# Kernel tuning notes

Measured on AMD Instinct MI355X. Metric: run time of the kernel, lower is better.

The kernel has to match this reference:

```python
import jax, jax.numpy as jnp
import numpy as np

N, E, H, IN, B, L, OUT = 50000, 600000, 128, 128, 256, 4, 10
BN_EPS = 1e-5


def setup_inputs() -> dict:
    key = jax.random.key(0)
    ks = jax.random.split(key, 12)
    x = jax.random.normal(ks[0], (N, IN), dtype=jnp.float32)
    edge_index = jax.random.randint(ks[1], (2, E), 0, N, dtype=jnp.int64)
    batch = jnp.sort(jax.random.randint(ks[2], (N,), 0, B, dtype=jnp.int64))
    s_in = 1.0 / np.sqrt(IN)
    s_h = 1.0 / np.sqrt(H)
    W_enc = jax.random.uniform(ks[3], (IN, H), jnp.float32, -s_in, s_in)
    b_enc = jax.random.uniform(ks[4], (H,), jnp.float32, -s_in, s_in)
    W = jax.random.uniform(ks[5], (L, H, H), jnp.float32, -s_h, s_h)
    b = jax.random.uniform(ks[6], (L, H), jnp.float32, -s_h, s_h)
    gamma = jnp.ones((L, H), jnp.float32)
    beta = jnp.zeros((L, H), jnp.float32)
    W_cls = jax.random.uniform(ks[7], (H, OUT), jnp.float32, -s_h, s_h)
    b_cls = jax.random.uniform(ks[8], (OUT,), jnp.float32, -s_h, s_h)
    return {"x": x, "edge_index": edge_index, "batch": batch,
            "W_enc": W_enc, "b_enc": b_enc, "W": W, "b": b,
            "gamma": gamma, "beta": beta, "W_cls": W_cls, "b_cls": b_cls}


def reference(x, edge_index, batch, W_enc, b_enc, W, b, gamma, beta, W_cls, b_cls):
    n = x.shape[0]
    # add self-loops (PyG GCNConv default)
    loop = jnp.arange(n, dtype=edge_index.dtype)
    row = jnp.concatenate([edge_index[0], loop])  # source nodes
    col = jnp.concatenate([edge_index[1], loop])  # target nodes
    # symmetric normalization: deg over targets, norm_e = d^-1/2[src] * d^-1/2[dst]
    deg = jax.ops.segment_sum(jnp.ones_like(col, dtype=x.dtype), col, num_segments=n)
    dinv = jnp.where(deg > 0, jax.lax.rsqrt(deg), 0.0)
    norm = dinv[row] * dinv[col]  # [E+N]

    # encoder (plain Linear since use_atom_encoder=False)
    h = x @ W_enc + b_enc

    for l in range(L):
        # GCNConv: transform, normalized scatter-add, bias
        t = h @ W[l]
        msg = norm[:, None] * t[row]               # [E+N, H] gather
        agg = jax.ops.segment_sum(msg, col, num_segments=n) + b[l]
        # BatchNorm1d (batch statistics, training-mode math)
        mean = jnp.mean(agg, axis=0)
        var = jnp.var(agg, axis=0)
        hn = (agg - mean) * jax.lax.rsqrt(var + BN_EPS) * gamma[l] + beta[l]
        h = jax.nn.relu(hn)  # dropout p=0.0 -> identity

    # global mean pool over graphs
    sums = jax.ops.segment_sum(h, batch, num_segments=B)
    counts = jax.ops.segment_sum(jnp.ones((n,), h.dtype), batch, num_segments=B)
    g = sums / jnp.maximum(counts, 1.0)[:, None]
    return g @ W_cls + b_cls
```

## Files before the change

### kernel.cpp

```cpp
#include <hip/hip_runtime.h>

#define NN 50000
#define NE 600000
#define HD 128
#define NL 4
#define NB 256
#define NO 10
#define BN_EPS 1e-5f

typedef short bf16x8 __attribute__((ext_vector_type(8)));
typedef float f32x4 __attribute__((ext_vector_type(4)));

__device__ __forceinline__ unsigned short f2bf(float f) {
    union { float f; unsigned int u; } x; x.f = f;
    unsigned int u = x.u;
    unsigned int r = (u + 0x7FFFu + ((u >> 16) & 1u)) >> 16;
    return (unsigned short)r;
}
__device__ __forceinline__ float bf2f(unsigned short s) {
    union { unsigned int u; float f; } x; x.u = ((unsigned int)s) << 16;
    return x.f;
}


__global__ void hist_kernel(const int* __restrict__ col, int* __restrict__ cnt, int e) {
    int i = blockIdx.x * blockDim.x + threadIdx.x;
    if (i < e) atomicAdd(&cnt[col[i]], 1);
}

__global__ void scan1_kernel(const int* __restrict__ cnt, int* __restrict__ outp,
                             int* __restrict__ bsums, float* __restrict__ dinv,
                             int M, int n) {
    __shared__ int s[256];
    int tid = threadIdx.x;
    int base = blockIdx.x * 1024 + tid * 4;
    int v[4];
#pragma unroll
    for (int j = 0; j < 4; ++j) {
        int idx = base + j;
        v[j] = (idx < n) ? cnt[idx] : 0;
        if (idx < n) dinv[idx] = rsqrtf((float)(v[j] + 1));
    }
    int tot = v[0] + v[1] + v[2] + v[3];
    s[tid] = tot;
    __syncthreads();
    for (int off = 1; off < 256; off <<= 1) {
        int x = (tid >= off) ? s[tid - off] : 0;
        __syncthreads();
        s[tid] += x;
        __syncthreads();
    }
    int run = (tid == 0) ? 0 : s[tid - 1];
#pragma unroll
    for (int j = 0; j < 4; ++j) {
        int idx = base + j;
        if (idx < M) outp[idx] = run;
        run += v[j];
    }
    if (tid == 255) bsums[blockIdx.x] = s[255];
}

__global__ void scan2_kernel(int* bsums, int nb) {
    if (threadIdx.x == 0 && blockIdx.x == 0) {
        int acc = 0;
        for (int i = 0; i < nb; ++i) { int v = bsums[i]; bsums[i] = acc; acc += v; }
    }
}

__global__ void scan3_kernel(int* __restrict__ outp, const int* __restrict__ bsums, int M) {
    int i = blockIdx.x * blockDim.x + threadIdx.x;
    if (i < M) outp[i] += bsums[i >> 10];
}

__global__ void place_kernel(const int* __restrict__ row, const int* __restrict__ col,
                             const float* __restrict__ dinv, const int* __restrict__ rp,
                             int* __restrict__ fill, int2* __restrict__ csr, int e) {
    int i = blockIdx.x * blockDim.x + threadIdx.x;
    if (i < e) {
        int r = row[i], c = col[i];
        int pos = atomicAdd(&fill[c], 1);
        int idx = rp[c] + pos;
        csr[idx] = make_int2(r, __float_as_int(dinv[r] * dinv[c]));
    }
}

__global__ void wconv_kernel(const float* __restrict__ W_enc, const float* __restrict__ W,
                             unsigned short* __restrict__ Wt) {
    int i = blockIdx.x * blockDim.x + threadIdx.x;
    if (i >= 5 * 16384) return;
    int m = i >> 14;
    int r = (i >> 7) & 127;
    int k = i & 127;
    const float* src = (m == 0) ? W_enc : (W + (size_t)(m - 1) * 16384);
    Wt[i] = f2bf(src[k * 128 + r]);
}

template <int AMODE>
__global__ __launch_bounds__(256) void gemm128_mfma(const void* __restrict__ Ap,
                                                    const unsigned short* __restrict__ Wt,
                                                    const float* __restrict__ bias,
                                                    const float* __restrict__ bnp,
                                                    unsigned short* __restrict__ Cp,
                                                    int nrows) {
    int wave = threadIdx.x >> 6;
    int lane = threadIdx.x & 63;
    int r16 = lane & 15;
    int kg = lane >> 4;
    int rowBase = blockIdx.x * 64 + wave * 16;
    int row = rowBase + r16;
    bool valid = row < nrows;

    bf16x8 afr[4];
#pragma unroll
    for (int s = 0; s < 4; ++s) {
        bf16x8 tt = {};
        int c0 = s * 32 + kg * 8;
        if constexpr (AMODE == 1) {
            const unsigned short* A = (const unsigned short*)Ap;
            if (valid) tt = *(const bf16x8*)&A[(size_t)row * 128 + c0];
        } else if constexpr (AMODE == 0) {
            const float* A = (const float*)Ap;
            if (valid) {
                const float* p = &A[(size_t)row * 128 + c0];
                float4 u0 = *(const float4*)p;
                float4 u1 = *(const float4*)(p + 4);
                tt[0] = (short)f2bf(u0.x); tt[1] = (short)f2bf(u0.y);
                tt[2] = (short)f2bf(u0.z); tt[3] = (short)f2bf(u0.w);
                tt[4] = (short)f2bf(u1.x); tt[5] = (short)f2bf(u1.y);
                tt[6] = (short)f2bf(u1.z); tt[7] = (short)f2bf(u1.w);
            }
        } else {
            const unsigned short* A = (const unsigned short*)Ap;
            if (valid) {
                bf16x8 raw = *(const bf16x8*)&A[(size_t)row * 128 + c0];
                float4 s0 = *(const float4*)&bnp[c0];
                float4 s1 = *(const float4*)&bnp[c0 + 4];
                float4 h0 = *(const float4*)&bnp[128 + c0];
                float4 h1 = *(const float4*)&bnp[128 + c0 + 4];
                tt[0] = (short)f2bf(fmaxf(bf2f((unsigned short)raw[0]) * s0.x + h0.x, 0.f));
                tt[1] = (short)f2bf(fmaxf(bf2f((unsigned short)raw[1]) * s0.y + h0.y, 0.f));
                tt[2] = (short)f2bf(fmaxf(bf2f((unsigned short)raw[2]) * s0.z + h0.z, 0.f));
                tt[3] = (short)f2bf(fmaxf(bf2f((unsigned short)raw[3]) * s0.w + h0.w, 0.f));
                tt[4] = (short)f2bf(fmaxf(bf2f((unsigned short)raw[4]) * s1.x + h1.x, 0.f));
                tt[5] = (short)f2bf(fmaxf(bf2f((unsigned short)raw[5]) * s1.y + h1.y, 0.f));
                tt[6] = (short)f2bf(fmaxf(bf2f((unsigned short)raw[6]) * s1.z + h1.z, 0.f));
                tt[7] = (short)f2bf(fmaxf(bf2f((unsigned short)raw[7]) * s1.w + h1.w, 0.f));
            }
        }
        afr[s] = tt;
    }

    f32x4 acc[8];
#pragma unroll
    for (int n = 0; n < 8; ++n) acc[n] = (f32x4){0.f, 0.f, 0.f, 0.f};

#pragma unroll
    for (int n = 0; n < 8; ++n) {
        const unsigned short* wp = &Wt[(size_t)(n * 16 + r16) * 128 + kg * 8];
#pragma unroll
        for (int s = 0; s < 4; ++s) {
            bf16x8 bfr = *(const bf16x8*)&wp[s * 32];
            acc[n] = __builtin_amdgcn_mfma_f32_16x16x32_bf16(afr[s], bfr, acc[n], 0, 0, 0);
        }
    }

#pragma unroll
    for (int n = 0; n < 8; ++n) {
        int col = n * 16 + r16;
        float bv = bias ? bias[col] : 0.f;
#pragma unroll
        for (int i = 0; i < 4; ++i) {
            int orow = rowBase + kg * 4 + i;
            if (orow < nrows)
                Cp[(size_t)orow * 128 + col] = f2bf(acc[n][i] + bv);
        }
    }
}

__global__ __launch_bounds__(256) void aggregate_kernel(const unsigned short* __restrict__ t,
                                                        const int* __restrict__ rp,
                                                        const int2* __restrict__ csr,
                                                        const float* __restrict__ dinv,
                                                        const float* __restrict__ bvec,
                                                        unsigned short* __restrict__ aggb, int n) {
    int wid = blockIdx.x * 4 + (threadIdx.x >> 6);
    int lane = threadIdx.x & 63;
    if (wid >= n) return;
    int c = lane * 2;
    float di = dinv[wid];
    float sw = di * di;
    unsigned int u = *(const unsigned int*)&t[(size_t)wid * 128 + c];
    float ax = sw * bf2f((unsigned short)(u & 0xffff)) + bvec[c];
    float ay = sw * bf2f((unsigned short)(u >> 16)) + bvec[c + 1];
    int e = rp[wid], e1 = rp[wid + 1];
    for (; e + 7 < e1; e += 8) {
        int2 ew[8];
        unsigned int uu[8];
#pragma unroll
        for (int j = 0; j < 8; ++j) ew[j] = csr[e + j];
#pragma unroll
        for (int j = 0; j < 8; ++j) uu[j] = *(const unsigned int*)&t[(size_t)ew[j].x * 128 + c];
#pragma unroll
        for (int j = 0; j < 8; ++j) {
            float w = __int_as_float(ew[j].y);
            ax += w * bf2f((unsigned short)(uu[j] & 0xffff));
            ay += w * bf2f((unsigned short)(uu[j] >> 16));
        }
    }
    for (; e + 3 < e1; e += 4) {
        int2 ew[4];
        unsigned int uu[4];
#pragma unroll
        for (int j = 0; j < 4; ++j) ew[j] = csr[e + j];
#pragma unroll
        for (int j = 0; j < 4; ++j) uu[j] = *(const unsigned int*)&t[(size_t)ew[j].x * 128 + c];
#pragma unroll
        for (int j = 0; j < 4; ++j) {
            float w = __int_as_float(ew[j].y);
            ax += w * bf2f((unsigned short)(uu[j] & 0xffff));
            ay += w * bf2f((unsigned short)(uu[j] >> 16));
        }
    }
    for (; e < e1; ++e) {
        int2 ew = csr[e];
        unsigned int u0 = *(const unsigned int*)&t[(size_t)ew.x * 128 + c];
        float w0 = __int_as_float(ew.y);
        ax += w0 * bf2f((unsigned short)(u0 & 0xffff));
        ay += w0 * bf2f((unsigned short)(u0 >> 16));
    }
    unsigned int o = (unsigned int)f2bf(ax) | ((unsigned int)f2bf(ay) << 16);
    *(unsigned int*)&aggb[(size_t)wid * 128 + c] = o;
}

#define BN_BLOCKS 256
__global__ __launch_bounds__(512) void bn_stats1_kernel(const unsigned short* __restrict__ aggb,
                                                        float* __restrict__ partials, int n) {
    int tid = threadIdx.x;
    int c4 = tid & 31, rs = tid >> 5;
    f32x4 s = {0.f, 0.f, 0.f, 0.f}, q = {0.f, 0.f, 0.f, 0.f};
    for (int r = blockIdx.x * 16 + rs; r < n; r += BN_BLOCKS * 16) {
        ushort4 v4 = *(const ushort4*)&aggb[(size_t)r * 128 + c4 * 4];
        f32x4 v = {bf2f(v4.x), bf2f(v4.y), bf2f(v4.z), bf2f(v4.w)};
        s += v;
        q += v * v;
    }
    __shared__ f32x4 ls[512], lq[512];
    ls[tid] = s;
    lq[tid] = q;
    __syncthreads();
    if (tid < 32) {
        f32x4 ss = ls[tid], qq = lq[tid];
#pragma unroll
        for (int j = 1; j < 16; ++j) { ss += ls[tid + 32 * j]; qq += lq[tid + 32 * j]; }
        float* pb = partials + (size_t)blockIdx.x * 256;
        *(f32x4*)&pb[tid * 4] = ss;
        *(f32x4*)&pb[128 + tid * 4] = qq;
    }
}

__global__ __launch_bounds__(256) void bn_stats2_kernel(const float* __restrict__ partials,
                                                        const float* __restrict__ gamma,
                                                        const float* __restrict__ beta,
                                                        float* __restrict__ bnp, float fn) {
    int tid = threadIdx.x;
    int col4 = tid & 63, g = tid >> 6;
    f32x4 acc = {0.f, 0.f, 0.f, 0.f};
#pragma unroll 8
    for (int bb = g; bb < BN_BLOCKS; bb += 4)
        acc += *(const f32x4*)&partials[(size_t)bb * 256 + col4 * 4];
    __shared__ f32x4 redv[256];
    __shared__ float red[256];
    redv[tid] = acc;
    __syncthreads();
    if (tid < 64) {
        f32x4 tot = redv[tid] + redv[tid + 64] + redv[tid + 128] + redv[tid + 192];
        *(f32x4*)&red[tid * 4] = tot;
    }
    __syncthreads();
    if (tid < 128) {
        float mean = red[tid] / fn;
        float var = fmaxf(red[128 + tid] / fn - mean * mean, 0.f);
        float sc = gamma[tid] * rsqrtf(var + BN_EPS);
        bnp[tid] = sc;
        bnp[128 + tid] = beta[tid] - mean * sc;
    }
}

__global__ __launch_bounds__(256) void pool_cls_kernel(const unsigned short* __restrict__ aggb,
                                                       const float* __restrict__ bnp,
                                                       const int* __restrict__ batch,
                                                       const float* __restrict__ Wc,
                                                       const float* __restrict__ bc,
                                                       float* __restrict__ out, int n) {
    int b = blockIdx.x;
    int tid = threadIdx.x;
    int lo = 0, hi = n;
    while (lo < hi) { int mid = (lo + hi) >> 1; if (batch[mid] < b) lo = mid + 1; else hi = mid; }
    int start = lo;
    hi = n;
    while (lo < hi) { int mid = (lo + hi) >> 1; if (batch[mid] <= b) lo = mid + 1; else hi = mid; }
    int end = lo;

    int c4 = tid & 31, rs = tid >> 5;
    f32x4 sc = *(const f32x4*)&bnp[c4 * 4];
    f32x4 sh = *(const f32x4*)&bnp[128 + c4 * 4];
    f32x4 acc = {0.f, 0.f, 0.f, 0.f};
    for (int r = start + rs; r < end; r += 8) {
        ushort4 v4 = *(const ushort4*)&aggb[(size_t)r * 128 + c4 * 4];
        f32x4 v = {bf2f(v4.x), bf2f(v4.y), bf2f(v4.z), bf2f(v4.w)};
        f32x4 y = v * sc + sh;
#pragma unroll
        for (int k = 0; k < 4; ++k) y[k] = fmaxf(y[k], 0.f);
        acc += y;
    }
    __shared__ f32x4 ls[256];
    __shared__ float g[128];
    ls[tid] = acc;
    __syncthreads();
    if (tid < 32) {
        f32x4 ss = ls[tid];
#pragma unroll
        for (int j = 1; j < 8; ++j) ss += ls[tid + 32 * j];
        float invc = 1.0f / fmaxf((float)(end - start), 1.0f);
#pragma unroll
        for (int k = 0; k < 4; ++k) g[tid * 4 + k] = ss[k] * invc;
    }
    __syncthreads();
    if (tid < NO) {
        float s = bc[tid];
        for (int c = 0; c < 128; ++c) s += g[c] * Wc[c * NO + tid];
        out[b * NO + tid] = s;
    }
}

extern "C" void kernel_launch(void* const* d_in, const int* in_sizes, int n_in,
                              void* d_out, int out_size, void* d_ws, size_t ws_size,
                              hipStream_t stream) {
    const float* x      = (const float*)d_in[0];
    const int*   eidx   = (const int*)d_in[1];
    const int*   batch  = (const int*)d_in[2];
    const float* W_enc  = (const float*)d_in[3];
    const float* b_enc  = (const float*)d_in[4];
    const float* W      = (const float*)d_in[5];
    const float* b      = (const float*)d_in[6];
    const float* gamma  = (const float*)d_in[7];
    const float* beta   = (const float*)d_in[8];
    const float* W_cls  = (const float*)d_in[9];
    const float* b_cls  = (const float*)d_in[10];
    float* out = (float*)d_out;

    const int* erow = eidx;
    const int* ecol = eidx + NE;

    float* dinv     = (float*)d_ws;
    float* partials = dinv + NN;
    float* bnp      = partials + BN_BLOCKS * 256;
    int2*  csr      = (int2*)(bnp + 256);
    unsigned short* h    = (unsigned short*)(csr + NE);
    unsigned short* t    = h + (size_t)NN * HD;
    unsigned short* aggb = t + (size_t)NN * HD;
    unsigned short* Wt   = aggb + (size_t)NN * HD;
    int* cnt      = (int*)(Wt + 5 * 16384);
    int* fill     = cnt + NN;
    int* rp       = fill + NN;
    int* bsums    = rp + NN + 1;

    hipMemsetAsync(cnt, 0, 2 * NN * sizeof(int), stream);

    hist_kernel<<<(NE + 255) / 256, 256, 0, stream>>>(ecol, cnt, NE);
    int M = NN + 1;
    int nscan = (M + 1023) / 1024;
    scan1_kernel<<<nscan, 256, 0, stream>>>(cnt, rp, bsums, dinv, M, NN);
    scan2_kernel<<<1, 64, 0, stream>>>(bsums, nscan);
    scan3_kernel<<<(M + 255) / 256, 256, 0, stream>>>(rp, bsums, M);
    place_kernel<<<(NE + 255) / 256, 256, 0, stream>>>(erow, ecol, dinv, rp, fill, csr, NE);

    wconv_kernel<<<(5 * 16384 + 255) / 256, 256, 0, stream>>>(W_enc, W, Wt);

    int gemmBlocks = (NN + 63) / 64;
    gemm128_mfma<0><<<gemmBlocks, 256, 0, stream>>>(x, Wt, b_enc, nullptr, h, NN);

    for (int l = 0; l < NL; ++l) {
        if (l == 0)
            gemm128_mfma<1><<<gemmBlocks, 256, 0, stream>>>(
                h, Wt + (size_t)(l + 1) * 16384, nullptr, nullptr, t, NN);
        else
            gemm128_mfma<2><<<gemmBlocks, 256, 0, stream>>>(
                aggb, Wt + (size_t)(l + 1) * 16384, nullptr, bnp, t, NN);
        aggregate_kernel<<<(NN + 3) / 4, 256, 0, stream>>>(t, rp, csr, dinv,
                                                           b + (size_t)l * HD, aggb, NN);
        bn_stats1_kernel<<<BN_BLOCKS, 512, 0, stream>>>(aggb, partials, NN);
        bn_stats2_kernel<<<1, 256, 0, stream>>>(partials, gamma + (size_t)l * HD,
                                                beta + (size_t)l * HD, bnp, (float)NN);
    }

    pool_cls_kernel<<<NB, 256, 0, stream>>>(aggb, bnp, batch, W_cls, b_cls, out, NN);
}
```

Baseline: 394.6 us.

## Fold encoder into first GCN weight, merge scan passes, vectorize GEMM stores

Precomputes W_enc·W0 and b_enc·W0 on device so the encoder linear and the layer-0 transform run as one GEMM, removing a full 50k×128 GEMM pass and the intermediate h buffer. The single-thread scan2 kernel is removed and each scan3 block now reduces the preceding block sums itself. The GEMM swaps MFMA operand order so each lane holds four consecutive output columns of one row and writes them as one ushort4 store. The algebraic fold changes bf16 rounding points slightly, since the product is rounded once instead of rounding h first.

Result: faster. 368.1 us (-6.7%).

```diff
diff --git a/kernel.cpp b/kernel.cpp
--- a/kernel.cpp
+++ b/kernel.cpp
@@ -60,16 +60,26 @@
     if (tid == 255) bsums[blockIdx.x] = s[255];
 }
 
-__global__ void scan2_kernel(int* bsums, int nb) {
-    if (threadIdx.x == 0 && blockIdx.x == 0) {
-        int acc = 0;
-        for (int i = 0; i < nb; ++i) { int v = bsums[i]; bsums[i] = acc; acc += v; }
-    }
-}
-
 __global__ void scan3_kernel(int* __restrict__ outp, const int* __restrict__ bsums, int M) {
-    int i = blockIdx.x * blockDim.x + threadIdx.x;
-    if (i < M) outp[i] += bsums[i >> 10];
+    __shared__ int sb[64];
+    int tid = threadIdx.x;
+    int seg = blockIdx.x >> 2;
+    if (tid < 64) sb[tid] = (tid < seg) ? bsums[tid] : 0;
+    __syncthreads();
+    if (tid < 32) sb[tid] += sb[tid + 32];
+    __syncthreads();
+    if (tid < 16) sb[tid] += sb[tid + 16];
+    __syncthreads();
+    if (tid < 8) sb[tid] += sb[tid + 8];
+    __syncthreads();
+    if (tid < 4) sb[tid] += sb[tid + 4];
+    __syncthreads();
+    if (tid < 2) sb[tid] += sb[tid + 2];
+    __syncthreads();
+    if (tid == 0) sb[0] += sb[1];
+    __syncthreads();
+    int i = blockIdx.x * 256 + tid;
+    if (i < M) outp[i] += sb[0];
 }
 
 __global__ void place_kernel(const int* __restrict__ row, const int* __restrict__ col,
@@ -84,15 +94,32 @@
     }
 }
 
-__global__ void wconv_kernel(const float* __restrict__ W_enc, const float* __restrict__ W,
-                             unsigned short* __restrict__ Wt) {
+__global__ void wconv_kernel(const float* __restrict__ W, unsigned short* __restrict__ Wt) {
     int i = blockIdx.x * blockDim.x + threadIdx.x;
-    if (i >= 5 * 16384) return;
+    if (i >= 4 * 16384) return;
     int m = i >> 14;
     int r = (i >> 7) & 127;
     int k = i & 127;
-    const float* src = (m == 0) ? W_enc : (W + (size_t)(m - 1) * 16384);
-    Wt[i] = f2bf(src[k * 128 + r]);
+    Wt[16384 + i] = f2bf(W[(size_t)m * 16384 + k * 128 + r]);
+}
+
+__global__ void fuse_enc_kernel(const float* __restrict__ W_enc, const float* __restrict__ W0,
+                                const float* __restrict__ b_enc,
+                                unsigned short* __restrict__ WtK, float* __restrict__ bb) {
+    if (blockIdx.x < 64) {
+        int gid = blockIdx.x * 256 + threadIdx.x;
+        int i = gid & 127, o = gid >> 7;
+        float s = 0.f;
+#pragma unroll 8
+        for (int h = 0; h < 128; ++h) s += W_enc[i * 128 + h] * W0[h * 128 + o];
+        WtK[o * 128 + i] = f2bf(s);
+    } else if (threadIdx.x < 128) {
+        int o = threadIdx.x;
+        float s = 0.f;
+#pragma unroll 8
+        for (int h = 0; h < 128; ++h) s += b_enc[h] * W0[h * 128 + o];
+        bb[o] = s;
+    }
 }
 
 template <int AMODE>
@@ -159,20 +186,23 @@
         const unsigned short* wp = &Wt[(size_t)(n * 16 + r16) * 128 + kg * 8];
 #pragma unroll
         for (int s = 0; s < 4; ++s) {
-            bf16x8 bfr = *(const bf16x8*)&wp[s * 32];
-            acc[n] = __builtin_amdgcn_mfma_f32_16x16x32_bf16(afr[s], bfr, acc[n], 0, 0, 0);
+            bf16x8 wfr = *(const bf16x8*)&wp[s * 32];
+            acc[n] = __builtin_amdgcn_mfma_f32_16x16x32_bf16(wfr, afr[s], acc[n], 0, 0, 0);
         }
     }
 
-#pragma unroll
-    for (int n = 0; n < 8; ++n) {
-        int col = n * 16 + r16;
-        float bv = bias ? bias[col] : 0.f;
-#pragma unroll
-        for (int i = 0; i < 4; ++i) {
-            int orow = rowBase + kg * 4 + i;
-            if (orow < nrows)
-                Cp[(size_t)orow * 128 + col] = f2bf(acc[n][i] + bv);
+    if (valid) {
+#pragma unroll
+        for (int n = 0; n < 8; ++n) {
+            int cbase = n * 16 + kg * 4;
+            float4 bv = make_float4(0.f, 0.f, 0.f, 0.f);
+            if (bias) bv = *(const float4*)&bias[cbase];
+            ushort4 o;
+            o.x = f2bf(acc[n][0] + bv.x);
+            o.y = f2bf(acc[n][1] + bv.y);
+            o.z = f2bf(acc[n][2] + bv.z);
+            o.w = f2bf(acc[n][3] + bv.w);
+            *(ushort4*)&Cp[(size_t)row * 128 + cbase] = o;
         }
     }
 }
@@ -355,9 +385,9 @@
     float* dinv     = (float*)d_ws;
     float* partials = dinv + NN;
     float* bnp      = partials + BN_BLOCKS * 256;
-    int2*  csr      = (int2*)(bnp + 256);
-    unsigned short* h    = (unsigned short*)(csr + NE);
-    unsigned short* t    = h + (size_t)NN * HD;
+    float* bb       = bnp + 256;
+    int2*  csr      = (int2*)(bb + 128);
+    unsigned short* t    = (unsigned short*)(csr + NE);
     unsigned short* aggb = t + (size_t)NN * HD;
     unsigned short* Wt   = aggb + (size_t)NN * HD;
     int* cnt      = (int*)(Wt + 5 * 16384);
@@ -371,20 +401,17 @@
     int M = NN + 1;
     int nscan = (M + 1023) / 1024;
     scan1_kernel<<<nscan, 256, 0, stream>>>(cnt, rp, bsums, dinv, M, NN);
-    scan2_kernel<<<1, 64, 0, stream>>>(bsums, nscan);
     scan3_kernel<<<(M + 255) / 256, 256, 0, stream>>>(rp, bsums, M);
     place_kernel<<<(NE + 255) / 256, 256, 0, stream>>>(erow, ecol, dinv, rp, fill, csr, NE);
 
-    wconv_kernel<<<(5 * 16384 + 255) / 256, 256, 0, stream>>>(W_enc, W, Wt);
+    wconv_kernel<<<(4 * 16384 + 255) / 256, 256, 0, stream>>>(W, Wt);
+    fuse_enc_kernel<<<65, 256, 0, stream>>>(W_enc, W, b_enc, Wt, bb);
 
     int gemmBlocks = (NN + 63) / 64;
-    gemm128_mfma<0><<<gemmBlocks, 256, 0, stream>>>(x, Wt, b_enc, nullptr, h, NN);
+    gemm128_mfma<0><<<gemmBlocks, 256, 0, stream>>>(x, Wt, bb, nullptr, t, NN);
 
     for (int l = 0; l < NL; ++l) {
-        if (l == 0)
-            gemm128_mfma<1><<<gemmBlocks, 256, 0, stream>>>(
-                h, Wt + (size_t)(l + 1) * 16384, nullptr, nullptr, t, NN);
-        else
+        if (l > 0)
             gemm128_mfma<2><<<gemmBlocks, 256, 0, stream>>>(
                 aggb, Wt + (size_t)(l + 1) * 16384, nullptr, bnp, t, NN);
         aggregate_kernel<<<(NN + 3) / 4, 256, 0, stream>>>(t, rp, csr, dinv,
```
